# Optimization experiments

Measured on AMD Instinct MI355X. Metric: run time of the kernel, lower is better.

Reference implementation:

```python
import jax, jax.numpy as jnp
import numpy as np

N_NODES = 100000
N_EDGES = 1600000
D_IN = 256
DIMS = (256, 256)


def setup_inputs() -> dict:
    key = jax.random.key(0)
    ks = jax.random.split(key, 10)
    inp = {
        "feat": jax.random.normal(ks[0], (N_NODES, D_IN), dtype=jnp.float32),
        "src": jax.random.randint(ks[1], (N_EDGES,), 0, N_NODES, dtype=jnp.int32),
        "dst": jax.random.randint(ks[2], (N_EDGES,), 0, N_NODES, dtype=jnp.int32),
    }
    # SAGEConv params per layer: fc_self, fc_neigh, bias (DGL mean aggregator)
    dims = (D_IN,) + tuple(DIMS)
    for l in range(len(DIMS)):
        fan_in, fan_out = dims[l], dims[l + 1]
        s = 1.0 / np.sqrt(fan_in)
        inp[f"W_self{l}"] = jax.random.uniform(ks[3 + 2 * l], (fan_in, fan_out), minval=-s, maxval=s, dtype=jnp.float32)
        inp[f"W_neigh{l}"] = jax.random.uniform(ks[4 + 2 * l], (fan_in, fan_out), minval=-s, maxval=s, dtype=jnp.float32)
        inp[f"b{l}"] = jnp.zeros((fan_out,), dtype=jnp.float32)
    return inp


def reference(feat, src, dst, W_self0, W_neigh0, b0, W_self1, W_neigh1, b1):
    N = feat.shape[0]
    # in-degree for mean aggregation; zero-degree nodes get 0 neighbor feature
    deg = jax.ops.segment_sum(jnp.ones_like(dst, dtype=feat.dtype), dst, num_segments=N)
    inv_deg = jnp.where(deg > 0, 1.0 / jnp.maximum(deg, 1.0), 0.0)[:, None]

    def sage(x, Ws, Wn, b):
        # gather src features, scatter-sum to dst, normalize by in-degree
        neigh = jax.ops.segment_sum(x[src], dst, num_segments=N) * inv_deg
        return x @ Ws + neigh @ Wn + b

    # eval mode: dropout is identity
    x0 = feat
    h1 = sage(x0, W_self0, W_neigh0, b0)
    a1 = jax.nn.relu(h1)  # activation + (identity) dropout between layers
    h2 = sage(a1, W_self1, W_neigh1, b1)
    # original returns [input, act(conv1), conv2]
    return (x0, a1, h2)
```

## Files before the change

### kernel.cpp

```cpp
#include <hip/hip_runtime.h>
#include <hip/hip_bf16.h>
#include <stdint.h>

#define NDIM 256

typedef __bf16 bf16_t;
typedef __bf16 bf16x8 __attribute__((ext_vector_type(8)));
typedef float f32x4 __attribute__((ext_vector_type(4)));

__device__ __forceinline__ float bf2f(uint16_t u) {
    union { uint32_t i; float f; } v; v.i = ((uint32_t)u) << 16; return v.f;
}
__device__ __forceinline__ uint16_t f2bf(float f) {
    union { float f; uint32_t i; } v; v.f = f;
    uint32_t r = v.i + 0x7fff + ((v.i >> 16) & 1);
    return (uint16_t)(r >> 16);
}


__global__ void k_deg(const int* __restrict__ dst, int* __restrict__ deg, int E) {
    int i = blockIdx.x * blockDim.x + threadIdx.x;
    if (i < E) atomicAdd(&deg[dst[i]], 1);
}

__global__ void k_partial(const int* __restrict__ deg, int* __restrict__ partial, int N) {
    __shared__ int sm[256];
    int i = blockIdx.x * 256 + threadIdx.x;
    sm[threadIdx.x] = (i < N) ? deg[i] : 0;
    __syncthreads();
    for (int s = 128; s > 0; s >>= 1) {
        if (threadIdx.x < s) sm[threadIdx.x] += sm[threadIdx.x + s];
        __syncthreads();
    }
    if (threadIdx.x == 0) partial[blockIdx.x] = sm[0];
}

__global__ void k_scan_partial(int* partial, int nb) {
    __shared__ int sm[512];
    int t = threadIdx.x;
    int v = (t < nb) ? partial[t] : 0;
    sm[t] = v;
    __syncthreads();
    for (int off = 1; off < 512; off <<= 1) {
        int u = (t >= off) ? sm[t - off] : 0;
        __syncthreads();
        sm[t] += u;
        __syncthreads();
    }
    if (t < nb) partial[t] = sm[t] - v;
}

__global__ void k_scan_block(const int* __restrict__ deg, const int* __restrict__ partial,
                             int* __restrict__ offsets, int* __restrict__ cursor,
                             float* __restrict__ invdeg, int N) {
    __shared__ int sm[256];
    int t = threadIdx.x;
    int i = blockIdx.x * 256 + t;
    int v = (i < N) ? deg[i] : 0;
    sm[t] = v;
    __syncthreads();
    for (int off = 1; off < 256; off <<= 1) {
        int u = (t >= off) ? sm[t - off] : 0;
        __syncthreads();
        sm[t] += u;
        __syncthreads();
    }
    if (i < N) {
        int excl = sm[t] - v + partial[blockIdx.x];
        offsets[i] = excl;
        cursor[i]  = excl;
        invdeg[i]  = (v > 0) ? (1.0f / (float)v) : 0.0f;
    }
}

__global__ void k_place(const int* __restrict__ src, const int* __restrict__ dst,
                        int* __restrict__ cursor, int* __restrict__ srcsorted, int E) {
    int i = blockIdx.x * blockDim.x + threadIdx.x;
    if (i < E) {
        int p = atomicAdd(&cursor[dst[i]], 1);
        srcsorted[p] = src[i];
    }
}


__global__ void k_cvt(const float4* __restrict__ in, ushort4* __restrict__ out, int n4) {
    int i = blockIdx.x * blockDim.x + threadIdx.x;
    if (i < n4) {
        float4 v = in[i];
        ushort4 o;
        o.x = f2bf(v.x); o.y = f2bf(v.y); o.z = f2bf(v.z); o.w = f2bf(v.w);
        out[i] = o;
    }
}

__global__ void k_wt(const float* __restrict__ W, uint16_t* __restrict__ Wt) {
    int n = blockIdx.x, k = threadIdx.x;
    Wt[n * NDIM + k] = f2bf(W[k * NDIM + n]);
}


__global__ __launch_bounds__(256) void k_aggr(
        const uint16_t* __restrict__ x, const int* __restrict__ srcsorted,
        const int* __restrict__ offsets, const int* __restrict__ deg,
        const float* __restrict__ invdeg, uint16_t* __restrict__ neigh, int N) {
    int node = blockIdx.x * 4 + (threadIdx.x >> 6);
    if (node >= N) return;
    int lane = threadIdx.x & 63;
    int beg = offsets[node];
    int d   = deg[node];
    float a0 = 0.f, a1 = 0.f, a2 = 0.f, a3 = 0.f;
    int j = 0;
    for (; j + 4 <= d; j += 4) {
        int s0 = srcsorted[beg + j + 0];
        int s1 = srcsorted[beg + j + 1];
        int s2 = srcsorted[beg + j + 2];
        int s3 = srcsorted[beg + j + 3];
        ushort4 v0 = *(const ushort4*)(x + (size_t)s0 * NDIM + lane * 4);
        ushort4 v1 = *(const ushort4*)(x + (size_t)s1 * NDIM + lane * 4);
        ushort4 v2 = *(const ushort4*)(x + (size_t)s2 * NDIM + lane * 4);
        ushort4 v3 = *(const ushort4*)(x + (size_t)s3 * NDIM + lane * 4);
        a0 += bf2f(v0.x) + bf2f(v1.x) + bf2f(v2.x) + bf2f(v3.x);
        a1 += bf2f(v0.y) + bf2f(v1.y) + bf2f(v2.y) + bf2f(v3.y);
        a2 += bf2f(v0.z) + bf2f(v1.z) + bf2f(v2.z) + bf2f(v3.z);
        a3 += bf2f(v0.w) + bf2f(v1.w) + bf2f(v2.w) + bf2f(v3.w);
    }
    for (; j < d; ++j) {
        int s = srcsorted[beg + j];
        ushort4 v = *(const ushort4*)(x + (size_t)s * NDIM + lane * 4);
        a0 += bf2f(v.x); a1 += bf2f(v.y); a2 += bf2f(v.z); a3 += bf2f(v.w);
    }
    float sc = invdeg[node];
    ushort4 o;
    o.x = f2bf(a0 * sc); o.y = f2bf(a1 * sc); o.z = f2bf(a2 * sc); o.w = f2bf(a3 * sc);
    *(ushort4*)(neigh + (size_t)node * NDIM + lane * 4) = o;
}


template <int RELU, int WB>
__global__ __launch_bounds__(256) void k_gemm(
        const uint16_t* __restrict__ A1, const uint16_t* __restrict__ B1t,
        const uint16_t* __restrict__ A2, const uint16_t* __restrict__ B2t,
        const float* __restrict__ bias, float* __restrict__ C,
        uint16_t* __restrict__ Cb, int M) {
    constexpr int LST = 40;
    __shared__ __align__(16) bf16_t As[128 * LST];
    __shared__ __align__(16) bf16_t Bs[128 * LST];
    int tid  = threadIdx.x;
    int w    = tid >> 6, lane = tid & 63;
    int wm   = w >> 1,   wn   = w & 1;
    int row0 = blockIdx.x * 128;
    int col0 = blockIdx.y * 128;

    f32x4 acc[4][4];
#pragma unroll
    for (int m = 0; m < 4; ++m)
#pragma unroll
        for (int n = 0; n < 4; ++n)
            acc[m][n] = (f32x4){0.f, 0.f, 0.f, 0.f};

    int r0s = tid >> 2, s0s = tid & 3;
    int r1s = r0s + 64, s1s = s0s;
    int kseg = lane >> 4;
    int rr   = lane & 15;

    for (int pair = 0; pair < 2; ++pair) {
        const uint16_t* A  = pair ? A2 : A1;
        const uint16_t* Bt = pair ? B2t : B1t;
        for (int k0 = 0; k0 < NDIM; k0 += 32) {
            int gra0 = min(row0 + r0s, M - 1);
            int gra1 = min(row0 + r1s, M - 1);
            uint4 va0 = *(const uint4*)(A  + (size_t)gra0 * NDIM + k0 + s0s * 8);
            uint4 va1 = *(const uint4*)(A  + (size_t)gra1 * NDIM + k0 + s1s * 8);
            uint4 vb0 = *(const uint4*)(Bt + (size_t)(col0 + r0s) * NDIM + k0 + s0s * 8);
            uint4 vb1 = *(const uint4*)(Bt + (size_t)(col0 + r1s) * NDIM + k0 + s1s * 8);
            __syncthreads();
            *(uint4*)(As + r0s * LST + s0s * 8) = va0;
            *(uint4*)(As + r1s * LST + s1s * 8) = va1;
            *(uint4*)(Bs + r0s * LST + s0s * 8) = vb0;
            *(uint4*)(Bs + r1s * LST + s1s * 8) = vb1;
            __syncthreads();

            bf16x8 af[4], bfr[4];
#pragma unroll
            for (int m = 0; m < 4; ++m)
                af[m] = *(const bf16x8*)(As + (wm * 64 + m * 16 + rr) * LST + kseg * 8);
#pragma unroll
            for (int n = 0; n < 4; ++n)
                bfr[n] = *(const bf16x8*)(Bs + (wn * 64 + n * 16 + rr) * LST + kseg * 8);
#pragma unroll
            for (int m = 0; m < 4; ++m)
#pragma unroll
                for (int n = 0; n < 4; ++n)
                    acc[m][n] = __builtin_amdgcn_mfma_f32_16x16x32_bf16(
                        af[m], bfr[n], acc[m][n], 0, 0, 0);
        }
    }

    int rbase = (lane >> 4) * 4;
    int cc    = lane & 15;
#pragma unroll
    for (int n = 0; n < 4; ++n) {
        int col = col0 + wn * 64 + n * 16 + cc;
        float bb = bias[col];
#pragma unroll
        for (int m = 0; m < 4; ++m) {
#pragma unroll
            for (int r = 0; r < 4; ++r) {
                int row = row0 + wm * 64 + m * 16 + rbase + r;
                if (row < M) {
                    float o = acc[m][n][r] + bb;
                    if (RELU) o = fmaxf(o, 0.f);
                    C[(size_t)row * NDIM + col] = o;
                    if (WB) Cb[(size_t)row * NDIM + col] = f2bf(o);
                }
            }
        }
    }
}

__global__ void k_copy(const float4* __restrict__ in, float4* __restrict__ out, int n4) {
    int i = blockIdx.x * blockDim.x + threadIdx.x;
    if (i < n4) out[i] = in[i];
}


extern "C" void kernel_launch(void* const* d_in, const int* in_sizes, int n_in,
                              void* d_out, int out_size, void* d_ws, size_t ws_size,
                              hipStream_t stream) {
    const float* feat = (const float*)d_in[0];
    const int*   src  = (const int*)d_in[1];
    const int*   dst  = (const int*)d_in[2];
    const float* Ws0  = (const float*)d_in[3];
    const float* Wn0  = (const float*)d_in[4];
    const float* b0   = (const float*)d_in[5];
    const float* Ws1  = (const float*)d_in[6];
    const float* Wn1  = (const float*)d_in[7];
    const float* b1   = (const float*)d_in[8];

    const int N = in_sizes[0] / NDIM;
    const int E = in_sizes[1];

    float* out    = (float*)d_out;
    float* out_x  = out;
    float* out_a1 = out + (size_t)N * NDIM;
    float* out_h2 = out + 2 * (size_t)N * NDIM;

    uint16_t* featb   = (uint16_t*)out_h2;
    uint16_t* neigh1b = (uint16_t*)out_h2 + (size_t)N * NDIM;
    uint16_t* a1b     = (uint16_t*)out_x;
    uint16_t* neigh2b = (uint16_t*)out_x + (size_t)N * NDIM;

    int*      deg       = (int*)d_ws;
    int*      offsets   = deg + N;
    int*      cursor    = offsets + N;
    float*    invdeg    = (float*)(cursor + N);
    int*      partial   = (int*)(invdeg + N);
    int*      srcsorted = partial + 512;
    uint16_t* Wt        = (uint16_t*)(srcsorted + E);
    uint16_t* Ws0t = Wt;
    uint16_t* Wn0t = Wt + 1 * NDIM * NDIM;
    uint16_t* Ws1t = Wt + 2 * NDIM * NDIM;
    uint16_t* Wn1t = Wt + 3 * NDIM * NDIM;

    hipMemsetAsync(deg, 0, (size_t)N * sizeof(int), stream);

    int nb = (N + 255) / 256;
    k_deg<<<(E + 255) / 256, 256, 0, stream>>>(dst, deg, E);
    k_partial<<<nb, 256, 0, stream>>>(deg, partial, N);
    k_scan_partial<<<1, 512, 0, stream>>>(partial, nb);
    k_scan_block<<<nb, 256, 0, stream>>>(deg, partial, offsets, cursor, invdeg, N);
    k_place<<<(E + 255) / 256, 256, 0, stream>>>(src, dst, cursor, srcsorted, E);

    k_wt<<<NDIM, NDIM, 0, stream>>>(Ws0, Ws0t);
    k_wt<<<NDIM, NDIM, 0, stream>>>(Wn0, Wn0t);
    k_wt<<<NDIM, NDIM, 0, stream>>>(Ws1, Ws1t);
    k_wt<<<NDIM, NDIM, 0, stream>>>(Wn1, Wn1t);

    int n4 = N * NDIM / 4;
    k_cvt<<<(n4 + 255) / 256, 256, 0, stream>>>((const float4*)feat, (ushort4*)featb, n4);

    dim3 gg((N + 127) / 128, NDIM / 128);

    k_aggr<<<(N + 3) / 4, 256, 0, stream>>>(featb, srcsorted, offsets, deg, invdeg, neigh1b, N);
    k_gemm<1, 1><<<gg, 256, 0, stream>>>(featb, Ws0t, neigh1b, Wn0t, b0, out_a1, a1b, N);

    k_aggr<<<(N + 3) / 4, 256, 0, stream>>>(a1b, srcsorted, offsets, deg, invdeg, neigh2b, N);
    k_gemm<0, 0><<<gg, 256, 0, stream>>>(a1b, Ws1t, neigh2b, Wn1t, b1, out_h2, nullptr, N);

    k_copy<<<(n4 + 255) / 256, 256, 0, stream>>>((const float4*)feat, (float4*)out_x, n4);
}
```

Before: 997.9 us.

## Restructure neighbor aggregation with shuffled indices and fuse conversion and copy kernels

The aggregation kernel now loads up to 64 neighbor indices per wave in one coalesced read and broadcasts them with shuffles. Each half-wave then handles a different edge using 16-byte loads, and the two halves' partial sums are combined with a shfl_xor at the end. The four weight-transpose launches are merged into one 2D launch. When the workspace is large enough, the bf16 staging buffers move into it, so the feature conversion and the output copy of x become a single pass. A leftover loop that loads values and discards them adds index loads and shuffles, unless the compiler removes it as dead code.

```diff
diff --git a/kernel.cpp b/kernel.cpp
--- a/kernel.cpp
+++ b/kernel.cpp
@@ -93,9 +93,26 @@
     }
 }
 
-__global__ void k_wt(const float* __restrict__ W, uint16_t* __restrict__ Wt) {
+__global__ void k_cvtcopy(const float4* __restrict__ in, float4* __restrict__ outf,
+                          ushort4* __restrict__ outb, int n4) {
+    int i = blockIdx.x * blockDim.x + threadIdx.x;
+    if (i < n4) {
+        float4 v = in[i];
+        outf[i] = v;
+        ushort4 o;
+        o.x = f2bf(v.x); o.y = f2bf(v.y); o.z = f2bf(v.z); o.w = f2bf(v.w);
+        outb[i] = o;
+    }
+}
+
+__global__ void k_wt4(const float* __restrict__ W0, const float* __restrict__ W1,
+                      const float* __restrict__ W2, const float* __restrict__ W3,
+                      uint16_t* __restrict__ Wt) {
+    int which = blockIdx.y;
+    const float* W = (which == 0) ? W0 : (which == 1) ? W1 : (which == 2) ? W2 : W3;
+    uint16_t* O = Wt + (size_t)which * NDIM * NDIM;
     int n = blockIdx.x, k = threadIdx.x;
-    Wt[n * NDIM + k] = f2bf(W[k * NDIM + n]);
+    O[n * NDIM + k] = f2bf(W[k * NDIM + n]);
 }
 
 
@@ -106,33 +123,57 @@
     int node = blockIdx.x * 4 + (threadIdx.x >> 6);
     if (node >= N) return;
     int lane = threadIdx.x & 63;
+    int half = lane >> 5;
+    int l32  = lane & 31;
     int beg = offsets[node];
     int d   = deg[node];
-    float a0 = 0.f, a1 = 0.f, a2 = 0.f, a3 = 0.f;
-    int j = 0;
-    for (; j + 4 <= d; j += 4) {
-        int s0 = srcsorted[beg + j + 0];
-        int s1 = srcsorted[beg + j + 1];
-        int s2 = srcsorted[beg + j + 2];
-        int s3 = srcsorted[beg + j + 3];
-        ushort4 v0 = *(const ushort4*)(x + (size_t)s0 * NDIM + lane * 4);
-        ushort4 v1 = *(const ushort4*)(x + (size_t)s1 * NDIM + lane * 4);
-        ushort4 v2 = *(const ushort4*)(x + (size_t)s2 * NDIM + lane * 4);
-        ushort4 v3 = *(const ushort4*)(x + (size_t)s3 * NDIM + lane * 4);
-        a0 += bf2f(v0.x) + bf2f(v1.x) + bf2f(v2.x) + bf2f(v3.x);
-        a1 += bf2f(v0.y) + bf2f(v1.y) + bf2f(v2.y) + bf2f(v3.y);
-        a2 += bf2f(v0.z) + bf2f(v1.z) + bf2f(v2.z) + bf2f(v3.z);
-        a3 += bf2f(v0.w) + bf2f(v1.w) + bf2f(v2.w) + bf2f(v3.w);
-    }
-    for (; j < d; ++j) {
-        int s = srcsorted[beg + j];
-        ushort4 v = *(const ushort4*)(x + (size_t)s * NDIM + lane * 4);
-        a0 += bf2f(v.x); a1 += bf2f(v.y); a2 += bf2f(v.z); a3 += bf2f(v.w);
-    }
-    float sc = invdeg[node];
-    ushort4 o;
-    o.x = f2bf(a0 * sc); o.y = f2bf(a1 * sc); o.z = f2bf(a2 * sc); o.w = f2bf(a3 * sc);
-    *(ushort4*)(neigh + (size_t)node * NDIM + lane * 4) = o;
+
+    float acc[8] = {0.f, 0.f, 0.f, 0.f, 0.f, 0.f, 0.f, 0.f};
+
+    for (int base = 0; base < d; base += 64) {
+        int rem = d - base; if (rem > 64) rem = 64;
+        int il = (lane < rem) ? srcsorted[beg + base + lane] : 0;
+#pragma unroll 4
+        for (int j = half; j < rem; j += 2) {
+            int s = __shfl(il, j);
+            ushort4 v = *(const ushort4*)(x + (size_t)s * NDIM + l32 * 8);
+            uint16_t e0 = v.x, e1 = v.y, e2 = v.z, e3 = v.w;
+            (void)e0; (void)e1; (void)e2; (void)e3;
+        }
+        break;
+    }
+
+    acc[0] = acc[1] = acc[2] = acc[3] = acc[4] = acc[5] = acc[6] = acc[7] = 0.f;
+    for (int base = 0; base < d; base += 64) {
+        int rem = d - base; if (rem > 64) rem = 64;
+        int il = (lane < rem) ? srcsorted[beg + base + lane] : 0;
+#pragma unroll 4
+        for (int j = half; j < rem; j += 2) {
+            int s = __shfl(il, j);
+            uint4 v = *(const uint4*)(x + (size_t)s * NDIM + l32 * 8);
+            acc[0] += bf2f((uint16_t)(v.x & 0xffff));
+            acc[1] += bf2f((uint16_t)(v.x >> 16));
+            acc[2] += bf2f((uint16_t)(v.y & 0xffff));
+            acc[3] += bf2f((uint16_t)(v.y >> 16));
+            acc[4] += bf2f((uint16_t)(v.z & 0xffff));
+            acc[5] += bf2f((uint16_t)(v.z >> 16));
+            acc[6] += bf2f((uint16_t)(v.w & 0xffff));
+            acc[7] += bf2f((uint16_t)(v.w >> 16));
+        }
+    }
+
+#pragma unroll
+    for (int c = 0; c < 8; ++c) acc[c] += __shfl_xor(acc[c], 32);
+
+    if (half == 0) {
+        float sc = invdeg[node];
+        uint4 o;
+        o.x = (uint32_t)f2bf(acc[0] * sc) | ((uint32_t)f2bf(acc[1] * sc) << 16);
+        o.y = (uint32_t)f2bf(acc[2] * sc) | ((uint32_t)f2bf(acc[3] * sc) << 16);
+        o.z = (uint32_t)f2bf(acc[4] * sc) | ((uint32_t)f2bf(acc[5] * sc) << 16);
+        o.w = (uint32_t)f2bf(acc[6] * sc) | ((uint32_t)f2bf(acc[7] * sc) << 16);
+        *(uint4*)(neigh + (size_t)node * NDIM + l32 * 8) = o;
+    }
 }
 
 
@@ -245,11 +286,6 @@
     float* out_a1 = out + (size_t)N * NDIM;
     float* out_h2 = out + 2 * (size_t)N * NDIM;
 
-    uint16_t* featb   = (uint16_t*)out_h2;
-    uint16_t* neigh1b = (uint16_t*)out_h2 + (size_t)N * NDIM;
-    uint16_t* a1b     = (uint16_t*)out_x;
-    uint16_t* neigh2b = (uint16_t*)out_x + (size_t)N * NDIM;
-
     int*      deg       = (int*)d_ws;
     int*      offsets   = deg + N;
     int*      cursor    = offsets + N;
@@ -258,9 +294,27 @@
     int*      srcsorted = partial + 512;
     uint16_t* Wt        = (uint16_t*)(srcsorted + E);
     uint16_t* Ws0t = Wt;
-    uint16_t* Wn0t = Wt + 1 * NDIM * NDIM;
-    uint16_t* Ws1t = Wt + 2 * NDIM * NDIM;
-    uint16_t* Wn1t = Wt + 3 * NDIM * NDIM;
+    uint16_t* Wn0t = Wt + 1 * (size_t)NDIM * NDIM;
+    uint16_t* Ws1t = Wt + 2 * (size_t)NDIM * NDIM;
+    uint16_t* Wn1t = Wt + 3 * (size_t)NDIM * NDIM;
+    uint16_t* wsbuf = Wt + 4 * (size_t)NDIM * NDIM;
+
+    size_t NK = (size_t)N * NDIM;
+    size_t need = ((char*)(wsbuf + 4 * NK)) - (char*)d_ws;
+    bool ws_ok = ws_size >= need;
+
+    uint16_t *featb, *neigh1b, *a1b, *neigh2b;
+    if (ws_ok) {
+        featb   = wsbuf;
+        neigh1b = wsbuf + NK;
+        a1b     = wsbuf + 2 * NK;
+        neigh2b = wsbuf + 3 * NK;
+    } else {
+        featb   = (uint16_t*)out_h2;
+        neigh1b = (uint16_t*)out_h2 + NK;
+        a1b     = (uint16_t*)out_x;
+        neigh2b = (uint16_t*)out_x + NK;
+    }
 
     hipMemsetAsync(deg, 0, (size_t)N * sizeof(int), stream);
 
@@ -271,13 +325,16 @@
     k_scan_block<<<nb, 256, 0, stream>>>(deg, partial, offsets, cursor, invdeg, N);
     k_place<<<(E + 255) / 256, 256, 0, stream>>>(src, dst, cursor, srcsorted, E);
 
-    k_wt<<<NDIM, NDIM, 0, stream>>>(Ws0, Ws0t);
-    k_wt<<<NDIM, NDIM, 0, stream>>>(Wn0, Wn0t);
-    k_wt<<<NDIM, NDIM, 0, stream>>>(Ws1, Ws1t);
-    k_wt<<<NDIM, NDIM, 0, stream>>>(Wn1, Wn1t);
+    dim3 gw(NDIM, 4);
+    k_wt4<<<gw, NDIM, 0, stream>>>(Ws0, Wn0, Ws1, Wn1, Wt);
 
     int n4 = N * NDIM / 4;
-    k_cvt<<<(n4 + 255) / 256, 256, 0, stream>>>((const float4*)feat, (ushort4*)featb, n4);
+    if (ws_ok) {
+        k_cvtcopy<<<(n4 + 255) / 256, 256, 0, stream>>>(
+            (const float4*)feat, (float4*)out_x, (ushort4*)featb, n4);
+    } else {
+        k_cvt<<<(n4 + 255) / 256, 256, 0, stream>>>((const float4*)feat, (ushort4*)featb, n4);
+    }
 
     dim3 gg((N + 127) / 128, NDIM / 128);
 
@@ -287,5 +344,7 @@
     k_aggr<<<(N + 3) / 4, 256, 0, stream>>>(a1b, srcsorted, offsets, deg, invdeg, neigh2b, N);
     k_gemm<0, 0><<<gg, 256, 0, stream>>>(a1b, Ws1t, neigh2b, Wn1t, b1, out_h2, nullptr, N);
 
-    k_copy<<<(n4 + 255) / 256, 256, 0, stream>>>((const float4*)feat, (float4*)out_x, n4);
-}
+    if (!ws_ok) {
+        k_copy<<<(n4 + 255) / 256, 256, 0, stream>>>((const float4*)feat, (float4*)out_x, n4);
+    }
+}
```

Measured after the change: 980.9 us. About the same (-1.7%).
